# Optimization experiments

Hardware: AMD Instinct MI355X
Metric: run time of the kernel (lower is better)

Reference implementation:

```python
import jax, jax.numpy as jnp
import numpy as np

NEG = -1e9


def _ln(x, g, b):
    m = x.mean(-1, keepdims=True)
    v = ((x - m) ** 2).mean(-1, keepdims=True)
    return (x - m) / jnp.sqrt(v + 1e-5) * g + b


def _block(single, pair, single_mask, pair_mask,
           pa_ln_g, pa_ln_b, pa_wqkv, pa_wg, pa_wout,
           pt_ln_g, pt_ln_b, pt_w1, pt_b1, pt_w2, pt_b2,
           sa_ln_g, sa_ln_b, sa_wq, sa_wkv, sa_wb, sa_wout,
           st_ln_g, st_ln_b, st_w1, st_b1, st_w2, st_b2):
    B, L, _, D = pair.shape
    H = sa_wb.shape[1]
    hd = D // H
    scale = 1.0 / jnp.sqrt(jnp.asarray(hd, dtype=pair.dtype))
    # ---- PairUpdate: PairAttention over L*L pseudo-tokens ----
    z = _ln(pair, pa_ln_g, pa_ln_b)                       # [B,L,L,D]
    N = L * L
    qkv = (z @ pa_wqkv).reshape(B, N, 3, H, hd)
    q = qkv[:, :, 0].transpose(0, 2, 1, 3)                # [B,H,N,hd]
    k = qkv[:, :, 1].transpose(0, 2, 1, 3)
    v = qkv[:, :, 2].transpose(0, 2, 1, 3)
    attn = jnp.einsum('bhid,bhjd->bhij', q, k) * scale    # [B,H,N,N]
    pm = pair_mask.reshape(B, 1, N)
    m = pm[:, :, :, None] * pm[:, :, None, :]             # [B,1,N,N]
    attn = jnp.where(m > 0, attn, NEG)
    attn = jax.nn.softmax(attn, axis=-1)
    out = jnp.einsum('bhij,bhjd->bhid', attn, v)          # [B,H,N,hd]
    out = out.transpose(0, 2, 1, 3).reshape(B, L, L, D)
    g = jax.nn.sigmoid(z @ pa_wg)
    out = (out @ pa_wout) * g * pair_mask[..., None]
    pair = pair + out
    t = _ln(pair, pt_ln_g, pt_ln_b)
    t = jax.nn.relu(t @ pt_w1 + pt_b1) @ pt_w2 + pt_b2
    pair = pair + t * pair_mask[..., None]
    # ---- SingleUpdate: AttentionPairBias ----
    s = _ln(single, sa_ln_g, sa_ln_b)                     # [B,L,D]
    q = (s @ sa_wq).reshape(B, L, H, hd)
    kv = (s @ sa_wkv).reshape(B, L, 2, H, hd)
    k2, v2 = kv[:, :, 0], kv[:, :, 1]
    attn = jnp.einsum('bihd,bjhd->bhij', q, k2) * scale   # [B,H,L,L]
    bias = (pair @ sa_wb).transpose(0, 3, 1, 2)           # [B,H,L,L]
    attn = attn + bias
    sm = single_mask[:, None, None, :]
    attn = jnp.where(sm > 0, attn, NEG)
    attn = jax.nn.softmax(attn, axis=-1)
    out = jnp.einsum('bhij,bjhd->bihd', attn, v2).reshape(B, L, D)
    single = single + (out @ sa_wout) * single_mask[..., None]
    # single transition
    t = _ln(single, st_ln_g, st_ln_b)
    t = jax.nn.relu(t @ st_w1 + st_b1) @ st_w2 + st_b2
    single = single + t * single_mask[..., None]
    return single, pair


def setup_inputs() -> dict:
    key = jax.random.key(0)
    B, L, D, H = 1, 64, 144, 8
    ks = iter(jax.random.split(key, 40))
    def nrm(shape, scale=0.02):
        return jax.random.normal(next(ks), shape, dtype=jnp.float32) * scale
    sm = jnp.ones((B, L), jnp.float32).at[:, L - 8:].set(0.0)
    pm = sm[:, :, None] * sm[:, None, :]
    return dict(
        single=jax.random.normal(next(ks), (B, L, D), jnp.float32),
        pair=jax.random.normal(next(ks), (B, L, L, D), jnp.float32),
        single_mask=sm,
        pair_mask=pm,
        pa_ln_g=jnp.ones((D,), jnp.float32), pa_ln_b=jnp.zeros((D,), jnp.float32),
        pa_wqkv=nrm((D, 3 * D)), pa_wg=nrm((D, D)), pa_wout=nrm((D, D)),
        pt_ln_g=jnp.ones((D,), jnp.float32), pt_ln_b=jnp.zeros((D,), jnp.float32),
        pt_w1=nrm((D, 4 * D)), pt_b1=jnp.zeros((4 * D,), jnp.float32),
        pt_w2=nrm((4 * D, D)), pt_b2=jnp.zeros((D,), jnp.float32),
        sa_ln_g=jnp.ones((D,), jnp.float32), sa_ln_b=jnp.zeros((D,), jnp.float32),
        sa_wq=nrm((D, D)), sa_wkv=nrm((D, 2 * D)), sa_wb=nrm((D, H)), sa_wout=nrm((D, D)),
        st_ln_g=jnp.ones((D,), jnp.float32), st_ln_b=jnp.zeros((D,), jnp.float32),
        st_w1=nrm((D, 4 * D)), st_b1=jnp.zeros((4 * D,), jnp.float32),
        st_w2=nrm((4 * D, D)), st_b2=jnp.zeros((D,), jnp.float32),
    )


def reference(single, pair, single_mask, pair_mask,
              pa_ln_g, pa_ln_b, pa_wqkv, pa_wg, pa_wout,
              pt_ln_g, pt_ln_b, pt_w1, pt_b1, pt_w2, pt_b2,
              sa_ln_g, sa_ln_b, sa_wq, sa_wkv, sa_wb, sa_wout,
              st_ln_g, st_ln_b, st_w1, st_b1, st_w2, st_b2):
    return _block(single, pair, single_mask, pair_mask,
                  pa_ln_g, pa_ln_b, pa_wqkv, pa_wg, pa_wout,
                  pt_ln_g, pt_ln_b, pt_w1, pt_b1, pt_w2, pt_b2,
                  sa_ln_g, sa_ln_b, sa_wq, sa_wkv, sa_wb, sa_wout,
                  st_ln_g, st_ln_b, st_w1, st_b1, st_w2, st_b2)
```

## Files before the change

### kernel.cpp

```cpp
#include <hip/hip_runtime.h>
#include <hip/hip_bf16.h>

typedef __hip_bfloat16 bf16;
typedef __attribute__((ext_vector_type(8))) short short8;
typedef __attribute__((ext_vector_type(16))) float floatx16;
typedef __attribute__((ext_vector_type(4))) unsigned int uint4v;

__device__ __forceinline__ float tof(bf16 x){ return __bfloat162float(x); }
__device__ __forceinline__ float bflo(unsigned u){ return __uint_as_float(u<<16); }
__device__ __forceinline__ float bfhi(unsigned u){ return __uint_as_float(u & 0xFFFF0000u); }
__device__ __forceinline__ float ldT(const void* p, long i, bool isf){
  return isf ? ((const float*)p)[i] : tof(((const bf16*)p)[i]);
}
__device__ __forceinline__ void stT(void* p, long i, bool isf, float v){
  if (isf) ((float*)p)[i] = v; else ((bf16*)p)[i] = __float2bfloat16(v);
}

#define LL 64
#define DD 144
#define NN 4096
#define HH 8
#define HDIM 18
#define SCALE 0.23570226039551584f
#define LOG2E 1.4426950408889634f

__global__ __launch_bounds__(256) void prep_weights(const unsigned* __restrict__ smaskw,
    int* __restrict__ dflag,
    const void* __restrict__ wqkv, const void* __restrict__ wg,
    const void* __restrict__ wout, const void* __restrict__ w1, const void* __restrict__ w2,
    const void* __restrict__ swq, const void* __restrict__ swkv,
    const void* __restrict__ swout, const void* __restrict__ sw1, const void* __restrict__ sw2,
    bf16* __restrict__ F1, bf16* __restrict__ Fout, bf16* __restrict__ Fw1,
    bf16* __restrict__ Fw2, bf16* __restrict__ Fs1, bf16* __restrict__ Wtswout,
    bf16* __restrict__ Wtst1, bf16* __restrict__ Wtst2){
  bool isf = (smaskw[0] == 0x3F800000u);
  if (blockIdx.x==0 && threadIdx.x==0) dflag[0] = isf ? 4 : 2;
  long t = (long)blockIdx.x*256 + threadIdx.x;
  if (t < 82944){
    int j=t&7, lane=(int)((t>>3)&63); long tk=t>>9; int ks=tk%9, tile=tk/9;
    int col=tile*32+(lane&31); int k=ks*16+(lane>>5)*8+j;
    float v = (col<432)? ldT(wqkv,(long)k*432+col,isf) : ldT(wg,(long)k*144+(col-432),isf);
    F1[t]=__float2bfloat16(v); return;
  } t -= 82944;
  if (t < 23040){
    int j=t&7, lane=(int)((t>>3)&63); long tk=t>>9; int ks=tk%9, tile=tk/9;
    int col=tile*32+(lane&31); if (col>143) col=143;
    int k=ks*16+(lane>>5)*8+j;
    Fout[t]=__float2bfloat16(ldT(wout,(long)k*144+col,isf)); return;
  } t -= 23040;
  if (t < 82944){
    int j=t&7, lane=(int)((t>>3)&63); long tk=t>>9; int ks=tk%9, tile=tk/9;
    int col=tile*32+(lane&31); int k=ks*16+(lane>>5)*8+j;
    Fw1[t]=__float2bfloat16(ldT(w1,(long)k*576+col,isf)); return;
  } t -= 82944;
  if (t < 92160){
    int j=t&7, lane=(int)((t>>3)&63); long tk=t>>9; int ks=tk%36, tile=tk/36;
    int col=tile*32+(lane&31); if (col>143) col=143;
    int k=ks*16+(lane>>5)*8+j;
    Fw2[t]=__float2bfloat16(ldT(w2,(long)k*144+col,isf)); return;
  } t -= 92160;
  if (t < 64512){
    int j=t&7, lane=(int)((t>>3)&63); long tk=t>>9; int ks=tk%9, tile=tk/9;
    int col=tile*32+(lane&31); if (col>431) col=431;
    int k=ks*16+(lane>>5)*8+j;
    float v = (col<144)? ldT(swq,(long)k*144+col,isf) : ldT(swkv,(long)k*288+(col-144),isf);
    Fs1[t]=__float2bfloat16(v); return;
  } t -= 64512;
  if (t < 20736){ int c=t/144,k=t-(long)c*144; Wtswout[t]=__float2bfloat16(ldT(swout,(long)k*144+c,isf)); return; }
  t -= 20736;
  if (t < 82944){ int c=t/144,k=t-(long)c*144; Wtst1[t]=__float2bfloat16(ldT(sw1,(long)k*576+c,isf)); return; }
  t -= 82944;
  if (t < 82944){ int c=t/576,k=t-(long)c*576; Wtst2[t]=__float2bfloat16(ldT(sw2,(long)k*144+c,isf)); return; }
}

__global__ __launch_bounds__(256) void gemm_fused1(const int* __restrict__ df,
    const void* __restrict__ pairv, const void* __restrict__ lng, const void* __restrict__ lnb,
    const bf16* __restrict__ F1,
    const void* __restrict__ pmask,
    bf16* __restrict__ Qb, bf16* __restrict__ Kf, bf16* __restrict__ Vf,
    bf16* __restrict__ gbuf,
    const void* __restrict__ singlev, const void* __restrict__ sag, const void* __restrict__ sab,
    const bf16* __restrict__ Fs1,
    bf16* __restrict__ q_sb, bf16* __restrict__ kv_sb){
  __shared__ short As[64*152];
  bool isf = df[0]==4;
  int tid=threadIdx.x, lane=tid&63, l31=lane&31, w=tid>>6, wr=w>>1, wc=w&1;
  int g=(lane>>5)*8;

  if (blockIdx.y == 64){
    if (blockIdx.x >= 7) return;
    for (int rr=w; rr<64; rr+=4){
      long base=(long)rr*DD;
      float e0=ldT(singlev,base+lane,isf), e1=ldT(singlev,base+lane+64,isf);
      float e2=(lane<16)?ldT(singlev,base+lane+128,isf):0.f;
      float s=e0+e1+e2;
      #pragma unroll
      for (int o=32;o;o>>=1) s += __shfl_xor(s,o);
      float mean=s*(1.f/144.f);
      float d0=e0-mean, d1=e1-mean, d2=(lane<16)?(e2-mean):0.f;
      float v=d0*d0+d1*d1+d2*d2;
      #pragma unroll
      for (int o=32;o;o>>=1) v += __shfl_xor(v,o);
      float rstd=rsqrtf(v*(1.f/144.f)+1e-5f);
      bf16 h0=__float2bfloat16(d0*rstd*ldT(sag,lane,isf)+ldT(sab,lane,isf));
      bf16 h1=__float2bfloat16(d1*rstd*ldT(sag,lane+64,isf)+ldT(sab,lane+64,isf));
      As[rr*152+lane]=*reinterpret_cast<short*>(&h0);
      As[rr*152+lane+64]=*reinterpret_cast<short*>(&h1);
      if (lane<16){
        bf16 h2=__float2bfloat16(d2*rstd*ldT(sag,lane+128,isf)+ldT(sab,lane+128,isf));
        As[rr*152+lane+128]=*reinterpret_cast<short*>(&h2);
      }
    }
    __syncthreads();
    int tile = blockIdx.x*2 + wc;
    const short8* wf = (const short8*)Fs1;
    floatx16 acc;
    #pragma unroll
    for (int i=0;i<16;i++) acc[i]=0.f;
    #pragma unroll
    for (int ks=0; ks<9; ks++){
      short8 af = *(const short8*)&As[(l31+32*wr)*152 + ks*16 + g];
      acc = __builtin_amdgcn_mfma_f32_32x32x16_bf16(af, wf[(tile*9+ks)*64+lane], acc, 0,0,0);
    }
    int col = tile*32 + l31;
    if (col < 432){
      #pragma unroll
      for (int r=0;r<16;r++){
        int row = 32*wr + (r&3)+8*(r>>2)+4*(lane>>5);
        if (col<144) q_sb[(size_t)row*DD+col] = __float2bfloat16(acc[r]);
        else kv_sb[(size_t)row*288+(col-144)] = __float2bfloat16(acc[r]);
      }
    }
    return;
  }

  int row0 = blockIdx.y*64, col0 = blockIdx.x*64;
  for (int rr=w; rr<64; rr+=4){
    long base=(long)(row0+rr)*DD;
    float e0=ldT(pairv,base+lane,isf), e1=ldT(pairv,base+lane+64,isf);
    float e2=(lane<16)?ldT(pairv,base+lane+128,isf):0.f;
    float s=e0+e1+e2;
    #pragma unroll
    for (int o=32;o;o>>=1) s += __shfl_xor(s,o);
    float mean=s*(1.f/144.f);
    float d0=e0-mean, d1=e1-mean, d2=(lane<16)?(e2-mean):0.f;
    float v=d0*d0+d1*d1+d2*d2;
    #pragma unroll
    for (int o=32;o;o>>=1) v += __shfl_xor(v,o);
    float rstd=rsqrtf(v*(1.f/144.f)+1e-5f);
    bf16 h0=__float2bfloat16(d0*rstd*ldT(lng,lane,isf)+ldT(lnb,lane,isf));
    bf16 h1=__float2bfloat16(d1*rstd*ldT(lng,lane+64,isf)+ldT(lnb,lane+64,isf));
    As[rr*152+lane]=*reinterpret_cast<short*>(&h0);
    As[rr*152+lane+64]=*reinterpret_cast<short*>(&h1);
    if (lane<16){
      bf16 h2=__float2bfloat16(d2*rstd*ldT(lng,lane+128,isf)+ldT(lnb,lane+128,isf));
      As[rr*152+lane+128]=*reinterpret_cast<short*>(&h2);
    }
  }
  __syncthreads();
  int tile = blockIdx.x*2 + wc;
  const short8* wf = (const short8*)F1;
  floatx16 acc;
  #pragma unroll
  for (int i=0;i<16;i++) acc[i]=0.f;
  #pragma unroll
  for (int ks=0; ks<9; ks++){
    short8 af = *(const short8*)&As[(l31+32*wr)*152 + ks*16 + g];
    acc = __builtin_amdgcn_mfma_f32_32x32x16_bf16(af, wf[(tile*9+ks)*64+lane], acc, 0,0,0);
  }
  int col = col0 + wc*32 + l31;
  #pragma unroll
  for (int r=0;r<16;r++){
    int row = row0 + 32*wr + (r&3)+8*(r>>2)+4*(lane>>5);
    if (col < 144){
      int hh = col/18, d = col - hh*18;
      Qb[((size_t)hh*NN+row)*32 + d] = __float2bfloat16(acc[r]*(SCALE*LOG2E));
    } else if (col < 288){
      int c2 = col-144, hh = c2/18, d = c2 - hh*18;
      int f = d>>4, rem = d&15, gs = rem>>3, j = rem&7;
      Kf[((((size_t)hh*128 + (row>>5))*2 + f)*64 + gs*32 + (row&31))*8 + j]
        = __float2bfloat16(acc[r]);
    } else if (col < 432){
      int c2 = col-288, hh = c2/18, d = c2 - hh*18;
      float pm = (ldT(pmask,row,isf)>0.f)?1.f:0.f;
      int kin = row&31, f = kin>>4, k15 = kin&15;
      int gs = (k15>>2)&1, j = (k15&3) | (((k15>>3)&1)<<2);
      Vf[((((size_t)hh*128 + (row>>5))*2 + f)*64 + gs*32 + d)*8 + j]
        = __float2bfloat16(acc[r]*pm);
    } else {
      int c2 = col-432;
      float gt = 1.f/(1.f+__expf(fminf(-acc[r],30.f)));
      gbuf[(size_t)row*DD+c2] = __float2bfloat16(gt);
    }
  }
  if (blockIdx.x==0){
    for (int t=threadIdx.x; t<64*8*7; t+=256){
      int n = row0 + t/56; int rem = t%56; int hh = rem/7, dw = rem%7 + 9;
      ((unsigned*)(Qb + ((size_t)hh*NN+n)*32))[dw] = 0;
    }
    for (int t=threadIdx.x; t<64*8; t+=256){
      int n = row0 + (t>>3), hh = t&7;
      float pm = (ldT(pmask,n,isf)>0.f)?1.f:0.f;
      int kin = n&31, f = kin>>4, k15 = kin&15;
      int gs = (k15>>2)&1, j = (k15&3) | (((k15>>3)&1)<<2);
      Vf[((((size_t)hh*128 + (n>>5))*2 + f)*64 + gs*32 + 18)*8 + j] = __float2bfloat16(pm);
    }
  }
}

__global__ __launch_bounds__(512) void pair_attn_mfma(const int* __restrict__ df,
    const bf16* __restrict__ Qb, const bf16* __restrict__ Kf,
    const bf16* __restrict__ Vf, bf16* __restrict__ aob){
  __shared__ float Comb[8][32][20];
  int h = blockIdx.x & 7, qp2 = blockIdx.x >> 3;
  int qtA = qp2*2, qtB = qp2*2+1;
  int tid = threadIdx.x;
  int w = tid >> 6, lane = tid & 63;
  int l31 = lane & 31, gsel = lane>>5;

  const unsigned* qpA = (const unsigned*)(Qb + ((size_t)h*NN + qtA*32 + l31)*32);
  const unsigned* qpB = (const unsigned*)(Qb + ((size_t)h*NN + qtB*32 + l31)*32);
  short8 qa0, qa1, qb0, qb1;
  #pragma unroll
  for (int j=0;j<4;j++){
    ((unsigned*)&qa0)[j] = qpA[gsel*4+j];
    ((unsigned*)&qa1)[j] = qpA[8+gsel*4+j];
    ((unsigned*)&qb0)[j] = qpB[gsel*4+j];
    ((unsigned*)&qb1)[j] = qpB[8+gsel*4+j];
  }

  floatx16 oA, oB;
  #pragma unroll
  for (int i=0;i<16;i++){ oA[i]=0.f; oB[i]=0.f; }

  const short8* kf8 = (const short8*)Kf + (size_t)h*16384;
  const short8* vf8 = (const short8*)Vf + (size_t)h*16384;
  int c0 = w*16;

  short8 af0 = kf8[(c0*2+0)*64 + lane];
  short8 af1 = kf8[(c0*2+1)*64 + lane];
  short8 av0 = vf8[(c0*2+0)*64 + lane];
  short8 av1 = vf8[(c0*2+1)*64 + lane];

  for (int cc=0; cc<16; cc++){
    int cn = c0 + (cc<15 ? cc+1 : 15);
    short8 naf0 = kf8[(cn*2+0)*64 + lane];
    short8 naf1 = kf8[(cn*2+1)*64 + lane];
    short8 nav0 = vf8[(cn*2+0)*64 + lane];
    short8 nav1 = vf8[(cn*2+1)*64 + lane];

    floatx16 s;
    short8 P1, P2;
    #pragma unroll
    for (int i=0;i<16;i++) s[i]=0.f;
    __builtin_amdgcn_s_setprio(1);
    s = __builtin_amdgcn_mfma_f32_32x32x16_bf16(af0, qa0, s, 0,0,0);
    s = __builtin_amdgcn_mfma_f32_32x32x16_bf16(af1, qa1, s, 0,0,0);
    __builtin_amdgcn_s_setprio(0);
    #pragma unroll
    for (int j=0;j<4;j++){
      unsigned e0 = __float_as_uint(__builtin_amdgcn_exp2f(s[2*j]));
      unsigned e1 = __float_as_uint(__builtin_amdgcn_exp2f(s[2*j+1]));
      ((unsigned*)&P1)[j] = __builtin_amdgcn_perm(e1, e0, 0x07060302);
      unsigned e2 = __float_as_uint(__builtin_amdgcn_exp2f(s[8+2*j]));
      unsigned e3 = __float_as_uint(__builtin_amdgcn_exp2f(s[9+2*j]));
      ((unsigned*)&P2)[j] = __builtin_amdgcn_perm(e3, e2, 0x07060302);
    }
    __builtin_amdgcn_s_setprio(1);
    oA = __builtin_amdgcn_mfma_f32_32x32x16_bf16(av0, P1, oA, 0,0,0);
    oA = __builtin_amdgcn_mfma_f32_32x32x16_bf16(av1, P2, oA, 0,0,0);
    __builtin_amdgcn_s_setprio(0);
    #pragma unroll
    for (int i=0;i<16;i++) s[i]=0.f;
    __builtin_amdgcn_s_setprio(1);
    s = __builtin_amdgcn_mfma_f32_32x32x16_bf16(af0, qb0, s, 0,0,0);
    s = __builtin_amdgcn_mfma_f32_32x32x16_bf16(af1, qb1, s, 0,0,0);
    __builtin_amdgcn_s_setprio(0);
    #pragma unroll
    for (int j=0;j<4;j++){
      unsigned e0 = __float_as_uint(__builtin_amdgcn_exp2f(s[2*j]));
      unsigned e1 = __float_as_uint(__builtin_amdgcn_exp2f(s[2*j+1]));
      ((unsigned*)&P1)[j] = __builtin_amdgcn_perm(e1, e0, 0x07060302);
      unsigned e2 = __float_as_uint(__builtin_amdgcn_exp2f(s[8+2*j]));
      unsigned e3 = __float_as_uint(__builtin_amdgcn_exp2f(s[9+2*j]));
      ((unsigned*)&P2)[j] = __builtin_amdgcn_perm(e3, e2, 0x07060302);
    }
    __builtin_amdgcn_s_setprio(1);
    oB = __builtin_amdgcn_mfma_f32_32x32x16_bf16(av0, P1, oB, 0,0,0);
    oB = __builtin_amdgcn_mfma_f32_32x32x16_bf16(av1, P2, oB, 0,0,0);
    __builtin_amdgcn_s_setprio(0);

    af0=naf0; af1=naf1; av0=nav0; av1=nav1;
  }

  #pragma unroll
  for (int r=0;r<16;r++){
    int d = (r&3) + 8*(r>>2) + 4*gsel;
    if (d < 20) Comb[w][l31][d] = oA[r];
  }
  __syncthreads();
  for (int t=tid; t<32*HDIM; t+=512){
    int q = t/HDIM, d = t-q*HDIM;
    float num = Comb[0][q][d]+Comb[1][q][d]+Comb[2][q][d]+Comb[3][q][d]
              + Comb[4][q][d]+Comb[5][q][d]+Comb[6][q][d]+Comb[7][q][d];
    float den = Comb[0][q][18]+Comb[1][q][18]+Comb[2][q][18]+Comb[3][q][18]
              + Comb[4][q][18]+Comb[5][q][18]+Comb[6][q][18]+Comb[7][q][18];
    aob[(size_t)(qtA*32+q)*DD + h*HDIM + d] = __float2bfloat16(num/fmaxf(den,1e-20f));
  }
  __syncthreads();
  #pragma unroll
  for (int r=0;r<16;r++){
    int d = (r&3) + 8*(r>>2) + 4*gsel;
    if (d < 20) Comb[w][l31][d] = oB[r];
  }
  __syncthreads();
  for (int t=tid; t<32*HDIM; t+=512){
    int q = t/HDIM, d = t-q*HDIM;
    float num = Comb[0][q][d]+Comb[1][q][d]+Comb[2][q][d]+Comb[3][q][d]
              + Comb[4][q][d]+Comb[5][q][d]+Comb[6][q][d]+Comb[7][q][d];
    float den = Comb[0][q][18]+Comb[1][q][18]+Comb[2][q][18]+Comb[3][q][18]
              + Comb[4][q][18]+Comb[5][q][18]+Comb[6][q][18]+Comb[7][q][18];
    aob[(size_t)(qtB*32+q)*DD + h*HDIM + d] = __float2bfloat16(num/fmaxf(den,1e-20f));
  }
}

__global__ __launch_bounds__(1024) void pair_tail(const int* __restrict__ df,
    const bf16* __restrict__ aob, const bf16* __restrict__ gbuf,
    const void* __restrict__ pairv, const void* __restrict__ pmaskv,
    const bf16* __restrict__ Fout, const void* __restrict__ ptln_g, const void* __restrict__ ptln_b,
    const bf16* __restrict__ Fw1, const void* __restrict__ b1v,
    const bf16* __restrict__ Fw2, const void* __restrict__ b2v,
    const void* __restrict__ wb, void* __restrict__ outP, long outOff,
    float* __restrict__ biasb){
  __shared__ __align__(16) char smem[65536];
  float* p1  = (float*)smem;
  short* ts  = (short*)(smem + 18432);
  short* hh_ = (short*)(smem + 28160);
  float* outv = (float*)(smem + 28160);

  bool isf = df[0]==4;
  int tid=threadIdx.x, lane=tid&63, l31=lane&31, gsel=lane>>5, g=gsel*8;
  int w=tid>>6;
  int r0 = blockIdx.x*32;
  const short8* foutf = (const short8*)Fout;
  const short8* fw1f  = (const short8*)Fw1;
  const short8* fw2f  = (const short8*)Fw2;

  for (int t=tid; t<32*72; t+=1024){
    int m=t/72, dw=t%72;
    ((unsigned*)ts)[m*76+dw] = ((const unsigned*)(aob + (size_t)(r0+m)*144))[dw];
  }
  __syncthreads();

  for (int tile=w; tile<5; tile+=16){
    int c0=tile*32;
    floatx16 acc;
    #pragma unroll
    for (int i=0;i<16;i++) acc[i]=0.f;
    #pragma unroll
    for (int ks=0; ks<9; ks++){
      short8 af = *(const short8*)&ts[l31*152 + ks*16 + g];
      acc = __builtin_amdgcn_mfma_f32_32x32x16_bf16(af, foutf[(tile*9+ks)*64+lane], acc, 0,0,0);
    }
    if (c0+l31 < 144){
      #pragma unroll
      for (int r=0;r<16;r++){
        int row=(r&3)+8*(r>>2)+4*gsel;
        p1[row*144 + c0+l31] = acc[r];
      }
    }
  }
  __syncthreads();
  for (int t=tid; t<32*144; t+=1024){
    int row=t/144; int col=t-row*144;
    long gidx=(long)(r0+row)*144 + col;
    float pm = (ldT(pmaskv, r0+row, isf)>0.f)?1.f:0.f;
    p1[t] = ldT(pairv,gidx,isf) + p1[t]*tof(gbuf[gidx])*pm;
  }
  __syncthreads();
  for (int rr=w; rr<32; rr+=16){
    float e0=p1[rr*144+lane], e1=p1[rr*144+lane+64], e2=(lane<16)?p1[rr*144+lane+128]:0.f;
    float s=e0+e1+e2;
    #pragma unroll
    for (int o=32;o;o>>=1) s += __shfl_xor(s,o);
    float mean=s*(1.f/144.f);
    float d0=e0-mean, d1=e1-mean, d2=(lane<16)?(e2-mean):0.f;
    float v=d0*d0+d1*d1+d2*d2;
    #pragma unroll
    for (int o=32;o;o>>=1) v += __shfl_xor(v,o);
    float rstd=rsqrtf(v*(1.f/144.f)+1e-5f);
    bf16 h0 = __float2bfloat16(d0*rstd*ldT(ptln_g,lane,isf)    + ldT(ptln_b,lane,isf));
    bf16 h1 = __float2bfloat16(d1*rstd*ldT(ptln_g,lane+64,isf) + ldT(ptln_b,lane+64,isf));
    ts[rr*152+lane]    = *reinterpret_cast<short*>(&h0);
    ts[rr*152+lane+64] = *reinterpret_cast<short*>(&h1);
    if (lane<16){
      bf16 h2 = __float2bfloat16(d2*rstd*ldT(ptln_g,lane+128,isf) + ldT(ptln_b,lane+128,isf));
      ts[rr*152+lane+128] = *reinterpret_cast<short*>(&h2);
    }
  }
  __syncthreads();
  for (int tile=w; tile<18; tile+=16){
    int c0=tile*32, colB=c0+l31;
    floatx16 acc;
    #pragma unroll
    for (int i=0;i<16;i++) acc[i]=0.f;
    #pragma unroll
    for (int ks=0; ks<9; ks++){
      short8 af = *(const short8*)&ts[l31*152 + ks*16 + g];
      acc = __builtin_amdgcn_mfma_f32_32x32x16_bf16(af, fw1f[(tile*9+ks)*64+lane], acc, 0,0,0);
    }
    float bb = ldT(b1v,colB,isf);
    #pragma unroll
    for (int r=0;r<16;r++){
      int row=(r&3)+8*(r>>2)+4*gsel;
      bf16 hv = __float2bfloat16(fmaxf(acc[r]+bb,0.f));
      hh_[row*584 + colB] = *reinterpret_cast<short*>(&hv);
    }
  }
  __syncthreads();
  floatx16 fin; int fc0 = -1;
  for (int tile=w; tile<5; tile+=16){
    int c0=tile*32;
    int colB=c0+l31; if (colB>143) colB=143;
    floatx16 acc;
    #pragma unroll
    for (int i=0;i<16;i++) acc[i]=0.f;
    #pragma unroll
    for (int ks=0; ks<36; ks++){
      short8 af = *(const short8*)&hh_[l31*584 + ks*16 + g];
      acc = __builtin_amdgcn_mfma_f32_32x32x16_bf16(af, fw2f[(tile*36+ks)*64+lane], acc, 0,0,0);
    }
    float bb = ldT(b2v,colB,isf);
    #pragma unroll
    for (int r=0;r<16;r++){
      int row=(r&3)+8*(r>>2)+4*gsel;
      float pm = (ldT(pmaskv, r0+row, isf)>0.f)?1.f:0.f;
      float val = p1[row*144 + colB] + (acc[r]+bb)*pm;
      if (c0+l31 < 144)
        stT(outP, outOff + (long)(r0+row)*144 + c0+l31, isf, val);
      fin[r]=val;
    }
    fc0 = c0;
  }
  __syncthreads();
  if (fc0 >= 0 && fc0+l31 < 144){
    #pragma unroll
    for (int r=0;r<16;r++){
      int row=(r&3)+8*(r>>2)+4*gsel;
      outv[row*144 + fc0+l31] = fin[r];
    }
  }
  __syncthreads();
  if (tid < 256){
    int n = tid>>3, hb = tid&7;
    float acc=0.f;
    #pragma unroll 4
    for (int k=0;k<144;k++) acc += outv[n*144+k]*ldT(wb,k*8+hb,isf);
    biasb[(size_t)(r0+n)*8+hb]=acc;
  }
}

__global__ __launch_bounds__(512) void single_tail(const int* __restrict__ df,
    const void* __restrict__ single, const bf16* __restrict__ q_sb,
    const bf16* __restrict__ kv_sb, const float* __restrict__ biasb,
    const void* __restrict__ smask, const bf16* __restrict__ Wtswout,
    const void* __restrict__ stln_g, const void* __restrict__ stln_b,
    const bf16* __restrict__ Wtst1, const void* __restrict__ st_b1,
    const bf16* __restrict__ Wtst2, const void* __restrict__ st_b2,
    void* __restrict__ outS){
  bool isf = df[0]==4;
  __shared__ __align__(16) short kvs[64*288];
  __shared__ float pexp[512];
  __shared__ float tot[8];
  __shared__ __align__(16) float bb[512];
  __shared__ float part[576];
  __shared__ float qs[DD], as_[DD], s1v[DD], tss[DD], hs[576];
  __shared__ float mr[2];
  int n = blockIdx.x, tid = threadIdx.x;
  {
    const uint4v* src = (const uint4v*)kv_sb;
    uint4v* dst = (uint4v*)kvs;
    for (int t=tid; t<2304; t+=512) dst[t] = src[t];
  }
  if (tid<DD) qs[tid] = tof(q_sb[(size_t)n*DD+tid]);
  {
    const uint4v* src = (const uint4v*)(biasb + (size_t)n*512);
    uint4v* dst = (uint4v*)bb;
    if (tid<128) dst[tid] = src[tid];
  }
  __syncthreads();
  {
    int h = tid>>6, j = tid&63;
    const unsigned* kr = (const unsigned*)&kvs[j*288 + h*HDIM];
    float s=0.f;
    #pragma unroll
    for (int i=0;i<9;i++){
      unsigned u = kr[i];
      s += qs[h*HDIM+2*i]*bflo(u) + qs[h*HDIM+2*i+1]*bfhi(u);
    }
    s = fminf(s*SCALE + bb[j*8+h], 30.f);
    pexp[tid] = (ldT(smask,j,isf)>0.f) ? __expf(s) : 0.f;
  }
  __syncthreads();
  if (tid<64){
    int h=tid>>3, j0=(tid&7)*8;
    float t2=0.f;
    #pragma unroll
    for (int j=0;j<8;j++) t2 += pexp[h*64+j0+j];
    #pragma unroll
    for (int o=4;o;o>>=1) t2 += __shfl_xor(t2,o);
    if ((tid&7)==0) tot[h] = fmaxf(t2,1e-20f);
  }
  __syncthreads();
  for (int t=tid; t<576; t+=512){
    int seg=t/144, d=t-seg*144, h=d/HDIM, j0=seg*16;
    float a0=0.f, a1=0.f;
    #pragma unroll
    for (int j=0;j<16;j+=2){
      unsigned u0 = ((unsigned)(unsigned short)kvs[(j0+j)*288 + 144 + d])<<16;
      unsigned u1 = ((unsigned)(unsigned short)kvs[(j0+j+1)*288 + 144 + d])<<16;
      a0 += pexp[h*64+j0+j]*__uint_as_float(u0);
      a1 += pexp[h*64+j0+j+1]*__uint_as_float(u1);
    }
    part[seg*144+d]=a0+a1;
  }
  __syncthreads();
  if (tid<DD){
    int h = tid/HDIM;
    as_[tid] = (part[tid]+part[144+tid]+part[288+tid]+part[432+tid])/tot[h];
  }
  __syncthreads();
  float sm = ldT(smask,n,isf);
  if (tid<288){
    int seg=tid/144, d=tid-seg*144;
    const uint4v* wr = (const uint4v*)(Wtswout + (size_t)d*DD) + seg*9;
    int b0=seg*72;
    float a=0.f;
    #pragma unroll
    for (int kw=0; kw<9; kw++){
      uint4v u = wr[kw]; int e=b0+8*kw;
      a += as_[e]*bflo(u[0]) + as_[e+1]*bfhi(u[0])
         + as_[e+2]*bflo(u[1]) + as_[e+3]*bfhi(u[1])
         + as_[e+4]*bflo(u[2]) + as_[e+5]*bfhi(u[2])
         + as_[e+6]*bflo(u[3]) + as_[e+7]*bfhi(u[3]);
    }
    part[seg*144+d]=a;
  }
  __syncthreads();
  if (tid<DD) s1v[tid] = ldT(single,(long)n*DD+tid,isf) + (part[tid]+part[144+tid])*sm;
  __syncthreads();
  if (tid < 64){
    float e0 = s1v[tid], e1 = s1v[tid+64], e2 = (tid<16)?s1v[tid+128]:0.f;
    float s = e0+e1+e2;
    #pragma unroll
    for (int o=32;o;o>>=1) s += __shfl_xor(s,o);
    float mean = s*(1.f/144.f);
    float d0=e0-mean, d1=e1-mean, d2=(tid<16)?(e2-mean):0.f;
    float v = d0*d0+d1*d1+d2*d2;
    #pragma unroll
    for (int o=32;o;o>>=1) v += __shfl_xor(v,o);
    if (tid==0){ mr[0]=mean; mr[1]=rsqrtf(v*(1.f/144.f)+1e-5f); }
  }
  __syncthreads();
  if (tid<DD) tss[tid] = (s1v[tid]-mr[0])*mr[1]*ldT(stln_g,tid,isf) + ldT(stln_b,tid,isf);
  __syncthreads();
  for (int c=tid; c<576; c+=512){
    const uint4v* wr = (const uint4v*)(Wtst1 + (size_t)c*DD);
    float a0=ldT(st_b1,c,isf), a1=0.f;
    #pragma unroll 3
    for (int kw=0; kw<18; kw+=2){
      uint4v u = wr[kw], u2 = wr[kw+1];
      a0 += tss[8*kw+0]*bflo(u[0]) + tss[8*kw+1]*bfhi(u[0])
          + tss[8*kw+2]*bflo(u[1]) + tss[8*kw+3]*bfhi(u[1])
          + tss[8*kw+4]*bflo(u[2]) + tss[8*kw+5]*bfhi(u[2])
          + tss[8*kw+6]*bflo(u[3]) + tss[8*kw+7]*bfhi(u[3]);
      a1 += tss[8*kw+8]*bflo(u2[0]) + tss[8*kw+9]*bfhi(u2[0])
          + tss[8*kw+10]*bflo(u2[1]) + tss[8*kw+11]*bfhi(u2[1])
          + tss[8*kw+12]*bflo(u2[2]) + tss[8*kw+13]*bfhi(u2[2])
          + tss[8*kw+14]*bflo(u2[3]) + tss[8*kw+15]*bfhi(u2[3]);
    }
    hs[c]=fmaxf(a0+a1,0.f);
  }
  __syncthreads();
  for (int t=tid; t<576; t+=512){
    int seg=t/144, d=t-seg*144;
    const uint4v* wr = (const uint4v*)(Wtst2 + (size_t)d*576) + seg*18;
    int b0=seg*144;
    float a0=0.f, a1=0.f;
    #pragma unroll 3
    for (int kw=0; kw<18; kw+=2){
      uint4v u = wr[kw], u2 = wr[kw+1];
      int e=b0+8*kw;
      a0 += hs[e]*bflo(u[0]) + hs[e+1]*bfhi(u[0])
          + hs[e+2]*bflo(u[1]) + hs[e+3]*bfhi(u[1])
          + hs[e+4]*bflo(u[2]) + hs[e+5]*bfhi(u[2])
          + hs[e+6]*bflo(u[3]) + hs[e+7]*bfhi(u[3]);
      a1 += hs[e+8]*bflo(u2[0]) + hs[e+9]*bfhi(u2[0])
          + hs[e+10]*bflo(u2[1]) + hs[e+11]*bfhi(u2[1])
          + hs[e+12]*bflo(u2[2]) + hs[e+13]*bfhi(u2[2])
          + hs[e+14]*bflo(u2[3]) + hs[e+15]*bfhi(u2[3]);
    }
    part[seg*144+d]=a0+a1;
  }
  __syncthreads();
  if (tid<DD)
    stT(outS,(long)n*DD+tid,isf,
        s1v[tid] + (ldT(st_b2,tid,isf)+part[tid]+part[144+tid]+part[288+tid]+part[432+tid])*sm);
}

extern "C" void kernel_launch(void* const* d_in, const int* in_sizes, int n_in,
                              void* d_out, int out_size, void* d_ws, size_t ws_size,
                              hipStream_t stream) {
  char* wsb = (char*)d_ws;
  int*   dflag = (int*)wsb;
  bf16*  F1     = (bf16*)(wsb + 16);
  bf16*  Fout   = F1 + 82944;
  bf16*  Fw1    = Fout + 23040;
  bf16*  Fw2    = Fw1 + 82944;
  bf16*  Fs1    = Fw2 + 92160;
  bf16*  Wtswout= Fs1 + 64512;
  bf16*  Wtst1  = Wtswout + 20736;
  bf16*  Wtst2  = Wtst1 + 82944;
  bf16*  Qb   = Wtst2 + 82944;
  bf16*  Kf   = Qb + (size_t)HH*NN*32;
  bf16*  Vf   = Kf + (size_t)HH*131072;
  bf16*  gbuf = Vf + (size_t)HH*131072;
  bf16*  aob  = gbuf + (size_t)NN*DD;
  float* biasb= (float*)(aob + (size_t)NN*DD);
  bf16*  q_sb = (bf16*)(biasb + NN*8);
  bf16*  kv_sb= q_sb + LL*DD;

  const long OUTP_OFF = (long)LL*DD;

  prep_weights<<<2079,256,0,stream>>>((const unsigned*)d_in[2], dflag,
      d_in[6], d_in[7], d_in[8], d_in[11], d_in[13],
      d_in[17], d_in[18], d_in[20], d_in[23], d_in[25],
      F1, Fout, Fw1, Fw2, Fs1, Wtswout, Wtst1, Wtst2);

  gemm_fused1<<<dim3(9,65),256,0,stream>>>(dflag, d_in[1], d_in[4], d_in[5], F1, d_in[3],
                                           Qb, Kf, Vf, gbuf,
                                           d_in[0], d_in[15], d_in[16], Fs1, q_sb, kv_sb);
  pair_attn_mfma<<<512,512,0,stream>>>(dflag, Qb, Kf, Vf, aob);
  pair_tail<<<128,1024,0,stream>>>(dflag, aob, gbuf, d_in[1], d_in[3],
                                   Fout, d_in[9], d_in[10], Fw1, d_in[12],
                                   Fw2, d_in[14], d_in[19], d_out, OUTP_OFF, biasb);
  single_tail<<<LL,512,0,stream>>>(dflag, d_in[0], q_sb, kv_sb, biasb, d_in[2],
                                   Wtswout, d_in[21], d_in[22], Wtst1, d_in[24],
                                   Wtst2, d_in[26], d_out);
  (void)in_sizes; (void)n_in; (void)out_size; (void)ws_size;
}
```

Measured before the change: 205.6 us.

## Move later-stage weight repacking into first GEMM launch and widen single tail

```diff
diff --git a/kernel.cpp b/kernel.cpp
--- a/kernel.cpp
+++ b/kernel.cpp
@@ -27,12 +27,8 @@
 __global__ __launch_bounds__(256) void prep_weights(const unsigned* __restrict__ smaskw,
     int* __restrict__ dflag,
     const void* __restrict__ wqkv, const void* __restrict__ wg,
-    const void* __restrict__ wout, const void* __restrict__ w1, const void* __restrict__ w2,
     const void* __restrict__ swq, const void* __restrict__ swkv,
-    const void* __restrict__ swout, const void* __restrict__ sw1, const void* __restrict__ sw2,
-    bf16* __restrict__ F1, bf16* __restrict__ Fout, bf16* __restrict__ Fw1,
-    bf16* __restrict__ Fw2, bf16* __restrict__ Fs1, bf16* __restrict__ Wtswout,
-    bf16* __restrict__ Wtst1, bf16* __restrict__ Wtst2){
+    bf16* __restrict__ F1, bf16* __restrict__ Fs1){
   bool isf = (smaskw[0] == 0x3F800000u);
   if (blockIdx.x==0 && threadIdx.x==0) dflag[0] = isf ? 4 : 2;
   long t = (long)blockIdx.x*256 + threadIdx.x;
@@ -42,35 +38,13 @@
     float v = (col<432)? ldT(wqkv,(long)k*432+col,isf) : ldT(wg,(long)k*144+(col-432),isf);
     F1[t]=__float2bfloat16(v); return;
   } t -= 82944;
-  if (t < 23040){
-    int j=t&7, lane=(int)((t>>3)&63); long tk=t>>9; int ks=tk%9, tile=tk/9;
-    int col=tile*32+(lane&31); if (col>143) col=143;
-    int k=ks*16+(lane>>5)*8+j;
-    Fout[t]=__float2bfloat16(ldT(wout,(long)k*144+col,isf)); return;
-  } t -= 23040;
-  if (t < 82944){
-    int j=t&7, lane=(int)((t>>3)&63); long tk=t>>9; int ks=tk%9, tile=tk/9;
-    int col=tile*32+(lane&31); int k=ks*16+(lane>>5)*8+j;
-    Fw1[t]=__float2bfloat16(ldT(w1,(long)k*576+col,isf)); return;
-  } t -= 82944;
-  if (t < 92160){
-    int j=t&7, lane=(int)((t>>3)&63); long tk=t>>9; int ks=tk%36, tile=tk/36;
-    int col=tile*32+(lane&31); if (col>143) col=143;
-    int k=ks*16+(lane>>5)*8+j;
-    Fw2[t]=__float2bfloat16(ldT(w2,(long)k*144+col,isf)); return;
-  } t -= 92160;
   if (t < 64512){
     int j=t&7, lane=(int)((t>>3)&63); long tk=t>>9; int ks=tk%9, tile=tk/9;
     int col=tile*32+(lane&31); if (col>431) col=431;
     int k=ks*16+(lane>>5)*8+j;
     float v = (col<144)? ldT(swq,(long)k*144+col,isf) : ldT(swkv,(long)k*288+(col-144),isf);
-    Fs1[t]=__float2bfloat16(v); return;
-  } t -= 64512;
-  if (t < 20736){ int c=t/144,k=t-(long)c*144; Wtswout[t]=__float2bfloat16(ldT(swout,(long)k*144+c,isf)); return; }
-  t -= 20736;
-  if (t < 82944){ int c=t/144,k=t-(long)c*144; Wtst1[t]=__float2bfloat16(ldT(sw1,(long)k*576+c,isf)); return; }
-  t -= 82944;
-  if (t < 82944){ int c=t/576,k=t-(long)c*576; Wtst2[t]=__float2bfloat16(ldT(sw2,(long)k*144+c,isf)); return; }
+    Fs1[t]=__float2bfloat16(v);
+  }
 }
 
 __global__ __launch_bounds__(256) void gemm_fused1(const int* __restrict__ df,
@@ -81,11 +55,42 @@
     bf16* __restrict__ gbuf,
     const void* __restrict__ singlev, const void* __restrict__ sag, const void* __restrict__ sab,
     const bf16* __restrict__ Fs1,
-    bf16* __restrict__ q_sb, bf16* __restrict__ kv_sb){
+    bf16* __restrict__ q_sb, bf16* __restrict__ kv_sb,
+    const void* __restrict__ wout, const void* __restrict__ w1, const void* __restrict__ w2,
+    const void* __restrict__ swout, const void* __restrict__ sw1, const void* __restrict__ sw2,
+    bf16* __restrict__ Fout, bf16* __restrict__ Fw1, bf16* __restrict__ Fw2,
+    bf16* __restrict__ Wtswout, bf16* __restrict__ Wtst1, bf16* __restrict__ Wtst2){
   __shared__ short As[64*152];
   bool isf = df[0]==4;
   int tid=threadIdx.x, lane=tid&63, l31=lane&31, w=tid>>6, wr=w>>1, wc=w&1;
   int g=(lane>>5)*8;
+
+  if (blockIdx.y >= 65){
+    long t = ((long)(blockIdx.y-65)*9 + blockIdx.x)*256 + threadIdx.x;
+    if (t < 23040){
+      int j=t&7, ln=(int)((t>>3)&63); long tk=t>>9; int ks=tk%9, tile=tk/9;
+      int col=tile*32+(ln&31); if (col>143) col=143;
+      int k=ks*16+(ln>>5)*8+j;
+      Fout[t]=__float2bfloat16(ldT(wout,(long)k*144+col,isf)); return;
+    } t -= 23040;
+    if (t < 82944){
+      int j=t&7, ln=(int)((t>>3)&63); long tk=t>>9; int ks=tk%9, tile=tk/9;
+      int col=tile*32+(ln&31); int k=ks*16+(ln>>5)*8+j;
+      Fw1[t]=__float2bfloat16(ldT(w1,(long)k*576+col,isf)); return;
+    } t -= 82944;
+    if (t < 92160){
+      int j=t&7, ln=(int)((t>>3)&63); long tk=t>>9; int ks=tk%36, tile=tk/36;
+      int col=tile*32+(ln&31); if (col>143) col=143;
+      int k=ks*16+(ln>>5)*8+j;
+      Fw2[t]=__float2bfloat16(ldT(w2,(long)k*144+col,isf)); return;
+    } t -= 92160;
+    if (t < 20736){ int c=t/144,k=t-(long)c*144; Wtswout[t]=__float2bfloat16(ldT(swout,(long)k*144+c,isf)); return; }
+    t -= 20736;
+    if (t < 82944){ int c=t/144,k=t-(long)c*144; Wtst1[t]=__float2bfloat16(ldT(sw1,(long)k*576+c,isf)); return; }
+    t -= 82944;
+    if (t < 82944){ int c=t/576,k=t-(long)c*576; Wtst2[t]=__float2bfloat16(ldT(sw2,(long)k*144+c,isf)); }
+    return;
+  }
 
   if (blockIdx.y == 64){
     if (blockIdx.x >= 7) return;
@@ -337,6 +342,7 @@
   short* ts  = (short*)(smem + 18432);
   short* hh_ = (short*)(smem + 28160);
   float* outv = (float*)(smem + 28160);
+  float* wbs  = (float*)(smem + 18432);
 
   bool isf = df[0]==4;
   int tid=threadIdx.x, lane=tid&63, l31=lane&31, gsel=lane>>5, g=gsel*8;
@@ -418,6 +424,7 @@
     }
   }
   __syncthreads();
+  for (int t=tid; t<1152; t+=1024) wbs[t] = ldT(wb, t, isf);
   floatx16 fin; int fc0 = -1;
   for (int tile=w; tile<5; tile+=16){
     int c0=tile*32;
@@ -455,12 +462,12 @@
     int n = tid>>3, hb = tid&7;
     float acc=0.f;
     #pragma unroll 4
-    for (int k=0;k<144;k++) acc += outv[n*144+k]*ldT(wb,k*8+hb,isf);
+    for (int k=0;k<144;k++) acc += outv[n*144+k]*wbs[k*8+hb];
     biasb[(size_t)(r0+n)*8+hb]=acc;
   }
 }
 
-__global__ __launch_bounds__(512) void single_tail(const int* __restrict__ df,
+__global__ __launch_bounds__(1024) void single_tail(const int* __restrict__ df,
     const void* __restrict__ single, const bf16* __restrict__ q_sb,
     const bf16* __restrict__ kv_sb, const float* __restrict__ biasb,
     const void* __restrict__ smask, const bf16* __restrict__ Wtswout,
@@ -473,14 +480,14 @@
   __shared__ float pexp[512];
   __shared__ float tot[8];
   __shared__ __align__(16) float bb[512];
-  __shared__ float part[576];
+  __shared__ float part[8*144];
   __shared__ float qs[DD], as_[DD], s1v[DD], tss[DD], hs[576];
   __shared__ float mr[2];
   int n = blockIdx.x, tid = threadIdx.x;
   {
     const uint4v* src = (const uint4v*)kv_sb;
     uint4v* dst = (uint4v*)kvs;
-    for (int t=tid; t<2304; t+=512) dst[t] = src[t];
+    for (int t=tid; t<2304; t+=1024) dst[t] = src[t];
   }
   if (tid<DD) qs[tid] = tof(q_sb[(size_t)n*DD+tid]);
   {
@@ -489,7 +496,7 @@
     if (tid<128) dst[tid] = src[tid];
   }
   __syncthreads();
-  {
+  if (tid < 512){
     int h = tid>>6, j = tid&63;
     const unsigned* kr = (const unsigned*)&kvs[j*288 + h*HDIM];
     float s=0.f;
@@ -512,11 +519,11 @@
     if ((tid&7)==0) tot[h] = fmaxf(t2,1e-20f);
   }
   __syncthreads();
-  for (int t=tid; t<576; t+=512){
-    int seg=t/144, d=t-seg*144, h=d/HDIM, j0=seg*16;
+  for (int t=tid; t<1152; t+=1024){
+    int seg=t/144, d=t-seg*144, h=d/HDIM, j0=seg*8;
     float a0=0.f, a1=0.f;
     #pragma unroll
-    for (int j=0;j<16;j+=2){
+    for (int j=0;j<8;j+=2){
       unsigned u0 = ((unsigned)(unsigned short)kvs[(j0+j)*288 + 144 + d])<<16;
       unsigned u1 = ((unsigned)(unsigned short)kvs[(j0+j+1)*288 + 144 + d])<<16;
       a0 += pexp[h*64+j0+j]*__uint_as_float(u0);
@@ -527,7 +534,9 @@
   __syncthreads();
   if (tid<DD){
     int h = tid/HDIM;
-    as_[tid] = (part[tid]+part[144+tid]+part[288+tid]+part[432+tid])/tot[h];
+    float su = part[tid]+part[144+tid]+part[288+tid]+part[432+tid]
+             + part[576+tid]+part[720+tid]+part[864+tid]+part[1008+tid];
+    as_[tid] = su/tot[h];
   }
   __syncthreads();
   float sm = ldT(smask,n,isf);
@@ -564,7 +573,8 @@
   __syncthreads();
   if (tid<DD) tss[tid] = (s1v[tid]-mr[0])*mr[1]*ldT(stln_g,tid,isf) + ldT(stln_b,tid,isf);
   __syncthreads();
-  for (int c=tid; c<576; c+=512){
+  if (tid<576){
+    int c=tid;
     const uint4v* wr = (const uint4v*)(Wtst1 + (size_t)c*DD);
     float a0=ldT(st_b1,c,isf), a1=0.f;
     #pragma unroll 3
@@ -582,13 +592,13 @@
     hs[c]=fmaxf(a0+a1,0.f);
   }
   __syncthreads();
-  for (int t=tid; t<576; t+=512){
+  for (int t=tid; t<1152; t+=1024){
     int seg=t/144, d=t-seg*144;
-    const uint4v* wr = (const uint4v*)(Wtst2 + (size_t)d*576) + seg*18;
-    int b0=seg*144;
+    const uint4v* wr = (const uint4v*)(Wtst2 + (size_t)d*576) + seg*9;
+    int b0=seg*72;
     float a0=0.f, a1=0.f;
-    #pragma unroll 3
-    for (int kw=0; kw<18; kw+=2){
+    #pragma unroll
+    for (int kw=0; kw<8; kw+=2){
       uint4v u = wr[kw], u2 = wr[kw+1];
       int e=b0+8*kw;
       a0 += hs[e]*bflo(u[0]) + hs[e+1]*bfhi(u[0])
@@ -600,12 +610,21 @@
           + hs[e+12]*bflo(u2[2]) + hs[e+13]*bfhi(u2[2])
           + hs[e+14]*bflo(u2[3]) + hs[e+15]*bfhi(u2[3]);
     }
+    {
+      uint4v u = wr[8]; int e=b0+64;
+      a0 += hs[e]*bflo(u[0]) + hs[e+1]*bfhi(u[0])
+          + hs[e+2]*bflo(u[1]) + hs[e+3]*bfhi(u[1])
+          + hs[e+4]*bflo(u[2]) + hs[e+5]*bfhi(u[2])
+          + hs[e+6]*bflo(u[3]) + hs[e+7]*bfhi(u[3]);
+    }
     part[seg*144+d]=a0+a1;
   }
   __syncthreads();
-  if (tid<DD)
-    stT(outS,(long)n*DD+tid,isf,
-        s1v[tid] + (ldT(st_b2,tid,isf)+part[tid]+part[144+tid]+part[288+tid]+part[432+tid])*sm);
+  if (tid<DD){
+    float su = part[tid]+part[144+tid]+part[288+tid]+part[432+tid]
+             + part[576+tid]+part[720+tid]+part[864+tid]+part[1008+tid];
+    stT(outS,(long)n*DD+tid,isf, s1v[tid] + (ldT(st_b2,tid,isf)+su)*sm);
+  }
 }
 
 extern "C" void kernel_launch(void* const* d_in, const int* in_sizes, int n_in,
@@ -632,20 +651,21 @@
 
   const long OUTP_OFF = (long)LL*DD;
 
-  prep_weights<<<2079,256,0,stream>>>((const unsigned*)d_in[2], dflag,
-      d_in[6], d_in[7], d_in[8], d_in[11], d_in[13],
-      d_in[17], d_in[18], d_in[20], d_in[23], d_in[25],
-      F1, Fout, Fw1, Fw2, Fs1, Wtswout, Wtst1, Wtst2);
-
-  gemm_fused1<<<dim3(9,65),256,0,stream>>>(dflag, d_in[1], d_in[4], d_in[5], F1, d_in[3],
-                                           Qb, Kf, Vf, gbuf,
-                                           d_in[0], d_in[15], d_in[16], Fs1, q_sb, kv_sb);
+  prep_weights<<<576,256,0,stream>>>((const unsigned*)d_in[2], dflag,
+      d_in[6], d_in[7], d_in[17], d_in[18], F1, Fs1);
+
+  gemm_fused1<<<dim3(9,232),256,0,stream>>>(dflag, d_in[1], d_in[4], d_in[5], F1, d_in[3],
+                                            Qb, Kf, Vf, gbuf,
+                                            d_in[0], d_in[15], d_in[16], Fs1, q_sb, kv_sb,
+                                            d_in[8], d_in[11], d_in[13],
+                                            d_in[20], d_in[23], d_in[25],
+                                            Fout, Fw1, Fw2, Wtswout, Wtst1, Wtst2);
   pair_attn_mfma<<<512,512,0,stream>>>(dflag, Qb, Kf, Vf, aob);
   pair_tail<<<128,1024,0,stream>>>(dflag, aob, gbuf, d_in[1], d_in[3],
                                    Fout, d_in[9], d_in[10], Fw1, d_in[12],
                                    Fw2, d_in[14], d_in[19], d_out, OUTP_OFF, biasb);
-  single_tail<<<LL,512,0,stream>>>(dflag, d_in[0], q_sb, kv_sb, biasb, d_in[2],
-                                   Wtswout, d_in[21], d_in[22], Wtst1, d_in[24],
-                                   Wtst2, d_in[26], d_out);
+  single_tail<<<LL,1024,0,stream>>>(dflag, d_in[0], q_sb, kv_sb, biasb, d_in[2],
+                                    Wtswout, d_in[21], d_in[22], Wtst1, d_in[24],
+                                    Wtst2, d_in[26], d_out);
   (void)in_sizes; (void)n_in; (void)out_size; (void)ws_size;
 }
```

Result: faster. 198.6 us (median of 3 runs) (-3.4%).
